# Kernel tuning notes

Hardware: AMD Instinct MI355X
Metric: run time of the kernel (lower is better)

## Reference

```python
import jax, jax.numpy as jnp
import numpy as np

L = 2        # gnn_layers
D = 256      # hidden_dim
E = 1024     # emb_dim
NCLS = 7
NEG = 1e30


def lstm_cell(x, h, c, Wih, Whh, bih, bhh):
    # torch.nn.LSTMCell math; gate order i, f, g, o
    g = x @ Wih.T + bih + h @ Whh.T + bhh
    i, f, gg, o = jnp.split(g, 4, axis=-1)
    c2 = jax.nn.sigmoid(f) * c + jax.nn.sigmoid(i) * jnp.tanh(gg)
    return jax.nn.sigmoid(o) * jnp.tanh(c2), c2


def dag_layer(Hl, adj_f, W1, W2, Wr, Wc_ih, Wc_hh, bc_ih, bc_hh, Wp_ih, Wp_hh, bp_ih, bp_hh):
    # Hl: (B,N,D). Sequential DAG recurrence with dot-product attention over growing prefix.
    B, N, Dh = Hl.shape
    zeros = jnp.zeros((B, Dh), Hl.dtype)
    h0 = Hl[:, 0]
    C0, _ = lstm_cell(h0, zeros, zeros, Wc_ih, Wc_hh, bc_ih, bc_hh)
    P0, _ = lstm_cell(zeros, h0, h0, Wp_ih, Wp_hh, bp_ih, bp_hh)
    Ht0 = C0 + P0
    # carry pre-projected keys/values incrementally to avoid O(N^2 D^2) work
    K2 = jnp.zeros((B, N, Dh), Hl.dtype).at[:, 0].set(Ht0 @ W2.T)
    Vr = jnp.zeros((B, N, Dh), Hl.dtype).at[:, 0].set(Ht0 @ Wr.T)
    H1 = jnp.zeros((B, N, Dh), Hl.dtype).at[:, 0].set(Ht0)
    pos = jnp.arange(N)

    def step(carry, i):
        K2, Vr, H1 = carry
        Q = jax.lax.dynamic_index_in_dim(Hl, i, axis=1, keepdims=False)      # (B,D)
        adj_i = jax.lax.dynamic_index_in_dim(adj_f, i, axis=1, keepdims=False)  # (B,N)
        q = Q @ W1.T
        logits = jnp.einsum('bd,bnd->bn', q, K2) - (1.0 - adj_i) * NEG  # mask_logic
        logits = jnp.where(pos[None, :] < i, logits, -NEG)              # only prefix :i
        w = jax.nn.softmax(logits, axis=-1)
        M = jnp.einsum('bn,bnd->bd', w, Vr)
        C, _ = lstm_cell(Q, M, M, Wc_ih, Wc_hh, bc_ih, bc_hh)
        P, _ = lstm_cell(M, Q, Q, Wp_ih, Wp_hh, bp_ih, bp_hh)
        Ht = C + P
        K2 = K2.at[:, i].set(Ht @ W2.T)
        Vr = Vr.at[:, i].set(Ht @ Wr.T)
        H1 = H1.at[:, i].set(Ht)
        return (K2, Vr, H1), None

    (K2, Vr, H1), _ = jax.lax.scan(step, (K2, Vr, H1), jnp.arange(1, N))
    return H1


def setup_inputs() -> dict:
    key = jax.random.key(0)
    ks = iter(jax.random.split(key, 40))
    B, N = 16, 128
    s = lambda *sh: jax.random.normal(next(ks), sh, jnp.float32) * 0.02
    in_dim = D * (L + 1) + E
    return dict(
        features=jax.random.normal(next(ks), (B, N, E), jnp.float32),
        adj=jnp.ones((B, N, N), jnp.int32),
        s_mask=jnp.zeros((B, N, N), jnp.int32),
        s_mask_onehot=jnp.zeros((B, N, N, 2), jnp.int32),
        lengths=jnp.ones((B,), jnp.int32) * N,
        fc1_W=s(D, E), fc1_b=jnp.zeros((D,), jnp.float32),
        W1=s(L, D, D), W2=s(L, D, D), Wr=s(L, D, D),
        Wc_ih=s(L, 4 * D, D), Wc_hh=s(L, 4 * D, D),
        bc_ih=jnp.zeros((L, 4 * D), jnp.float32), bc_hh=jnp.zeros((L, 4 * D), jnp.float32),
        Wp_ih=s(L, 4 * D, D), Wp_hh=s(L, 4 * D, D),
        bp_ih=jnp.zeros((L, 4 * D), jnp.float32), bp_hh=jnp.zeros((L, 4 * D), jnp.float32),
        m0_W=s(D, in_dim), m0_b=jnp.zeros((D,), jnp.float32),
        m1_W=s(D, D), m1_b=jnp.zeros((D,), jnp.float32),
        m2_W=s(NCLS, D), m2_b=jnp.zeros((NCLS,), jnp.float32),
    )


def reference(features, adj, s_mask, s_mask_onehot, lengths,
              fc1_W, fc1_b, W1, W2, Wr,
              Wc_ih, Wc_hh, bc_ih, bc_hh,
              Wp_ih, Wp_hh, bp_ih, bp_hh,
              m0_W, m0_b, m1_W, m1_b, m2_W, m2_b):
    # s_mask / s_mask_onehot unused for attn_type='dotprod', no_rel_attn=True
    # lengths unused for nodal_att_type=None (attentive_node_features is identity)
    adj_f = adj.astype(features.dtype)
    H0 = jax.nn.relu(features @ fc1_W.T + fc1_b)
    Hs = [H0]
    for l in range(L):
        Hs.append(dag_layer(Hs[l], adj_f,
                            W1[l], W2[l], Wr[l],
                            Wc_ih[l], Wc_hh[l], bc_ih[l], bc_hh[l],
                            Wp_ih[l], Wp_hh[l], bp_ih[l], bp_hh[l]))
    Hcat = jnp.concatenate(Hs + [features], axis=2)  # (B,N,D*(L+1)+E)
    h = jax.nn.relu(Hcat @ m0_W.T + m0_b)
    h = jax.nn.relu(h @ m1_W.T + m1_b)  # mlp_layers-1 extra layer; dropout p=0 -> identity
    return h @ m2_W.T + m2_b            # (B,N,num_class)
```

## Files before the change

### kernel.cpp

```cpp
#include <hip/hip_runtime.h>
#include <hip/hip_fp16.h>
#include <math.h>

#define B_ 16
#define N_ 128
#define D_ 256
#define E_ 1024
#define GD4 1024
#define SENT 0xFFC0DEADu

typedef _Float16 h2 __attribute__((ext_vector_type(2)));

template<bool BIAS, bool RELU>
__global__ __launch_bounds__(256) void gemm_k(const float* __restrict__ X,
    const float* __restrict__ W, const float* __restrict__ bias,
    float* __restrict__ C, int M, int N, int K)
{
  __shared__ float Xs[32][68];
  __shared__ float Ws[32][68];
  const int tid = threadIdx.x;
  const int m0 = blockIdx.x * 64, n0 = blockIdx.y * 64;
  const int tm = tid >> 4, tn = tid & 15;
  float acc[4][4] = {};
  for (int k0 = 0; k0 < K; k0 += 32) {
    for (int e = tid; e < 2048; e += 256) {
      int mm = e >> 5, kk = e & 31;
      Xs[kk][mm] = X[(m0+mm)*K + k0+kk];
    }
    for (int e = tid; e < 2048; e += 256) {
      int nn = e >> 5, kk = e & 31;
      Ws[kk][nn] = (n0+nn < N) ? W[(n0+nn)*K + k0+kk] : 0.f;
    }
    __syncthreads();
    for (int kk = 0; kk < 32; kk++) {
      float4 a = *(const float4*)&Xs[kk][tm*4];
      float4 b = *(const float4*)&Ws[kk][tn*4];
      acc[0][0] += a.x*b.x; acc[0][1] += a.x*b.y; acc[0][2] += a.x*b.z; acc[0][3] += a.x*b.w;
      acc[1][0] += a.y*b.x; acc[1][1] += a.y*b.y; acc[1][2] += a.y*b.z; acc[1][3] += a.y*b.w;
      acc[2][0] += a.z*b.x; acc[2][1] += a.z*b.y; acc[2][2] += a.z*b.z; acc[2][3] += a.z*b.w;
      acc[3][0] += a.w*b.x; acc[3][1] += a.w*b.y; acc[3][2] += a.w*b.z; acc[3][3] += a.w*b.w;
    }
    __syncthreads();
  }
  for (int i2 = 0; i2 < 4; i2++) {
    int row = m0 + tm*4 + i2;
    for (int j2 = 0; j2 < 4; j2++) {
      int col = n0 + tn*4 + j2;
      if (col < N) {
        float v = acc[i2][j2];
        if (BIAS) v += bias[col];
        if (RELU) v = fmaxf(v, 0.f);
        C[row*N + col] = v;
      }
    }
  }
}

__global__ __launch_bounds__(256) void prepamat_k(const float* __restrict__ W2,
    const float* __restrict__ W1, float* __restrict__ AM)
{
  __shared__ float Xs[32][68];
  __shared__ float Ws[32][68];
  const int tid = threadIdx.x;
  const int m0 = blockIdx.x * 64, n0 = blockIdx.y * 64;
  const float* X = W2 + blockIdx.z * 65536;
  const float* W = W1 + blockIdx.z * 65536;
  float* C = AM + blockIdx.z * 65536;
  const int tm = tid >> 4, tn = tid & 15;
  float acc[4][4] = {};
  for (int k0 = 0; k0 < 256; k0 += 32) {
    for (int e = tid; e < 2048; e += 256) {
      int kk = e >> 6, mm = e & 63;
      Xs[kk][mm] = X[(k0+kk)*256 + m0+mm];
    }
    for (int e = tid; e < 2048; e += 256) {
      int kk = e >> 6, nn = e & 63;
      Ws[kk][nn] = W[(k0+kk)*256 + n0+nn];
    }
    __syncthreads();
    for (int kk = 0; kk < 32; kk++) {
      float4 a = *(const float4*)&Xs[kk][tm*4];
      float4 b = *(const float4*)&Ws[kk][tn*4];
      acc[0][0] += a.x*b.x; acc[0][1] += a.x*b.y; acc[0][2] += a.x*b.z; acc[0][3] += a.x*b.w;
      acc[1][0] += a.y*b.x; acc[1][1] += a.y*b.y; acc[1][2] += a.y*b.z; acc[1][3] += a.y*b.w;
      acc[2][0] += a.z*b.x; acc[2][1] += a.z*b.y; acc[2][2] += a.z*b.z; acc[2][3] += a.z*b.w;
      acc[3][0] += a.w*b.x; acc[3][1] += a.w*b.y; acc[3][2] += a.w*b.z; acc[3][3] += a.w*b.w;
    }
    __syncthreads();
  }
  for (int i2 = 0; i2 < 4; i2++)
    for (int j2 = 0; j2 < 4; j2++)
      C[(m0 + tm*4 + i2)*256 + n0 + tn*4 + j2] = acc[i2][j2];
}

__global__ __launch_bounds__(256) void prepnn_k(const float* __restrict__ Wch,
    const float* __restrict__ Wpi, const float* __restrict__ Wr,
    float* __restrict__ OUT)
{
  __shared__ float Xs[32][68];
  __shared__ float Ws[32][68];
  const int tid = threadIdx.x;
  const int m0 = blockIdx.x * 64, n0 = blockIdx.y * 64;
  const int l = blockIdx.z;
  const float* X = (m0 < 1024) ? (Wch + l*262144 + m0*256)
                               : (Wpi + l*262144 + (m0-1024)*256);
  const float* W = Wr + l*65536;
  float* C = OUT + l*524288;
  const int tm = tid >> 4, tn = tid & 15;
  float acc[4][4] = {};
  for (int k0 = 0; k0 < 256; k0 += 32) {
    for (int e = tid; e < 2048; e += 256) {
      int mm = e >> 5, kk = e & 31;
      Xs[kk][mm] = X[mm*256 + k0+kk];
    }
    for (int e = tid; e < 2048; e += 256) {
      int kk = e >> 6, nn = e & 63;
      Ws[kk][nn] = W[(k0+kk)*256 + n0+nn];
    }
    __syncthreads();
    for (int kk = 0; kk < 32; kk++) {
      float4 a = *(const float4*)&Xs[kk][tm*4];
      float4 b = *(const float4*)&Ws[kk][tn*4];
      acc[0][0] += a.x*b.x; acc[0][1] += a.x*b.y; acc[0][2] += a.x*b.z; acc[0][3] += a.x*b.w;
      acc[1][0] += a.y*b.x; acc[1][1] += a.y*b.y; acc[1][2] += a.y*b.z; acc[1][3] += a.y*b.w;
      acc[2][0] += a.z*b.x; acc[2][1] += a.z*b.y; acc[2][2] += a.z*b.z; acc[2][3] += a.z*b.w;
      acc[3][0] += a.w*b.x; acc[3][1] += a.w*b.y; acc[3][2] += a.w*b.z; acc[3][3] += a.w*b.w;
    }
    __syncthreads();
  }
  for (int i2 = 0; i2 < 4; i2++)
    for (int j2 = 0; j2 < 4; j2++)
      C[(m0 + tm*4 + i2)*256 + n0 + tn*4 + j2] = acc[i2][j2];
}

__global__ void bias_sum_k(const float* __restrict__ bci, const float* __restrict__ bch,
                           const float* __restrict__ bpi, const float* __restrict__ bph,
                           float* __restrict__ bcC, float* __restrict__ bpC)
{
  int i = blockIdx.x*256 + threadIdx.x;
  if (i < 2048) { bcC[i] = bci[i] + bch[i]; bpC[i] = bpi[i] + bph[i]; }
}

__global__ void pack_k(const float* __restrict__ wchpi, const float* __restrict__ wr,
                       _Float16* __restrict__ out)
{
  int idx = blockIdx.x*256 + threadIdx.x;
  int l  = idx / 589824; int rem = idx % 589824;
  int sl = rem / 36864;  int rem2 = rem % 36864;
  int cq = rem2 / 1152;  int rem3 = rem2 % 1152;
  int r  = rem3 >> 3;    int e = rem3 & 7;
  int c  = cq*8 + e;
  int g  = r >> 4, dl = r & 15;
  int d  = sl*16 + dl;
  float v;
  if (g < 8) v = wchpi[l*524288 + (g*256 + d)*256 + c];
  else       v = wr[l*65536 + d*256 + c];
  out[idx] = (_Float16)v;
}

__global__ void fill_k(unsigned* __restrict__ a, unsigned* __restrict__ b)
{
  int i = blockIdx.x*256 + threadIdx.x;
  if (i < 524288) {
    __hip_atomic_store(a + i, SENT, __ATOMIC_RELAXED, __HIP_MEMORY_SCOPE_AGENT);
    __hip_atomic_store(b + i, SENT, __ATOMIC_RELAXED, __HIP_MEMORY_SCOPE_AGENT);
  }
}

__global__ __launch_bounds__(256) void prologue_k(const float* __restrict__ X,
    const float* __restrict__ Wc, const float* __restrict__ Wp,
    const float* __restrict__ Am, const float* __restrict__ bcc,
    const float* __restrict__ bpc, float* __restrict__ GQC,
    float* __restrict__ GQP, float* __restrict__ VM)
{
  __shared__ float Xs[32][68];
  __shared__ float Ws[32][68];
  const int tid = threadIdx.x;
  const int m0 = blockIdx.x * 64;
  const int nt = blockIdx.y;
  const float* W; const float* bias; float* C; int n0; int NC;
  if (nt < 16)      { W = Wc; bias = bcc;     C = GQC; n0 = nt*64;      NC = 1024; }
  else if (nt < 32) { W = Wp; bias = bpc;     C = GQP; n0 = (nt-16)*64; NC = 1024; }
  else              { W = Am; bias = nullptr; C = VM;  n0 = (nt-32)*64; NC = 256;  }
  const int tm = tid >> 4, tn = tid & 15;
  float acc[4][4] = {};
  for (int k0 = 0; k0 < 256; k0 += 32) {
    for (int e = tid; e < 2048; e += 256) {
      int mm = e >> 5, kk = e & 31;
      Xs[kk][mm] = X[(m0+mm)*256 + k0+kk];
    }
    for (int e = tid; e < 2048; e += 256) {
      int nn = e >> 5, kk = e & 31;
      Ws[kk][nn] = W[(n0+nn)*256 + k0+kk];
    }
    __syncthreads();
    for (int kk = 0; kk < 32; kk++) {
      float4 a = *(const float4*)&Xs[kk][tm*4];
      float4 b = *(const float4*)&Ws[kk][tn*4];
      acc[0][0] += a.x*b.x; acc[0][1] += a.x*b.y; acc[0][2] += a.x*b.z; acc[0][3] += a.x*b.w;
      acc[1][0] += a.y*b.x; acc[1][1] += a.y*b.y; acc[1][2] += a.y*b.z; acc[1][3] += a.y*b.w;
      acc[2][0] += a.z*b.x; acc[2][1] += a.z*b.y; acc[2][2] += a.z*b.z; acc[2][3] += a.z*b.w;
      acc[3][0] += a.w*b.x; acc[3][1] += a.w*b.y; acc[3][2] += a.w*b.z; acc[3][3] += a.w*b.w;
    }
    __syncthreads();
  }
  for (int i2 = 0; i2 < 4; i2++) {
    int row = m0 + tm*4 + i2;
    for (int j2 = 0; j2 < 4; j2++) {
      int col = n0 + tn*4 + j2;
      float v = acc[i2][j2];
      if (bias) v += bias[col];
      C[row*NC + col] = v;
    }
  }
}

__global__ __launch_bounds__(256) void m0fused_k(const float* __restrict__ H0,
    const float* __restrict__ H1, const float* __restrict__ H2,
    const float* __restrict__ feat, const float* __restrict__ W,
    const float* __restrict__ bias, float* __restrict__ C)
{
  __shared__ float Xs[32][68];
  __shared__ float Ws[32][68];
  const int tid = threadIdx.x;
  const int m0 = blockIdx.x * 64, n0 = blockIdx.y * 64;
  const int tm = tid >> 4, tn = tid & 15;
  float acc[4][4] = {};
  for (int k0 = 0; k0 < 1792; k0 += 32) {
    for (int e = tid; e < 2048; e += 256) {
      int mm = e >> 5, kk = e & 31;
      int k = k0 + kk, row = m0 + mm;
      float v;
      if (k < 768) {
        const float* src = (k < 256) ? H0 : ((k < 512) ? H1 : H2);
        v = src[row*256 + (k & 255)];
      } else v = feat[row*1024 + (k - 768)];
      Xs[kk][mm] = v;
    }
    for (int e = tid; e < 2048; e += 256) {
      int nn = e >> 5, kk = e & 31;
      Ws[kk][nn] = W[(n0+nn)*1792 + k0+kk];
    }
    __syncthreads();
    for (int kk = 0; kk < 32; kk++) {
      float4 a = *(const float4*)&Xs[kk][tm*4];
      float4 b = *(const float4*)&Ws[kk][tn*4];
      acc[0][0] += a.x*b.x; acc[0][1] += a.x*b.y; acc[0][2] += a.x*b.z; acc[0][3] += a.x*b.w;
      acc[1][0] += a.y*b.x; acc[1][1] += a.y*b.y; acc[1][2] += a.y*b.z; acc[1][3] += a.y*b.w;
      acc[2][0] += a.z*b.x; acc[2][1] += a.z*b.y; acc[2][2] += a.z*b.z; acc[2][3] += a.z*b.w;
      acc[3][0] += a.w*b.x; acc[3][1] += a.w*b.y; acc[3][2] += a.w*b.z; acc[3][3] += a.w*b.w;
    }
    __syncthreads();
  }
  for (int i2 = 0; i2 < 4; i2++) {
    int row = m0 + tm*4 + i2;
    for (int j2 = 0; j2 < 4; j2++) {
      int col = n0 + tn*4 + j2;
      C[row*256 + col] = fmaxf(acc[i2][j2] + bias[col], 0.f);
    }
  }
}

__device__ __forceinline__ float sigf(float x) { return 1.f / (1.f + __expf(-x)); }
__device__ __forceinline__ float tanhfast(float x) {
  float xc = fminf(fmaxf(x, -15.f), 15.f);
  float e = __expf(-2.f * xc);
  return (1.f - e) / (1.f + e);
}
__device__ __forceinline__ float dot2w(unsigned w, h2 hv, float acc) {
#if __has_builtin(__builtin_amdgcn_fdot2)
  return __builtin_amdgcn_fdot2(__builtin_bit_cast(h2, w), hv, acc, false);
#else
  union { unsigned u; _Float16 e[2]; } c; c.u = w;
  return acc + (float)c.e[0]*(float)hv.x + (float)c.e[1]*(float)hv.y;
#endif
}
__device__ __forceinline__ float dot2h(h2 a, h2 b, float acc) {
#if __has_builtin(__builtin_amdgcn_fdot2)
  return __builtin_amdgcn_fdot2(a, b, acc, false);
#else
  return acc + (float)a.x*(float)b.x + (float)a.y*(float)b.y;
#endif
}

__global__ __launch_bounds__(512, 2) void scan_k(
    const float* __restrict__ Hl,
    const float* __restrict__ Vm,
    const float* __restrict__ gqC,
    const float* __restrict__ gqP,
    const _Float16* __restrict__ WTp,
    const int*   __restrict__ adj,
    float* __restrict__ Hout)
{
  __shared__ uint4 wl4[4608];
  __shared__ float G[128*144];
  __shared__ __align__(16) _Float16 h2s[256];
  __shared__ float v_s[256];
  __shared__ __align__(16) _Float16 v2s[256];
  __shared__ float psum[128];
  __shared__ float aw[128];
  __shared__ int   adj_s[2][128];
  __shared__ float gqc_l[2][64], gqp_l[2][64];
  __shared__ float ql[2][16];
  __shared__ float Gg[144];
  __shared__ float red[2];

  const int tid = threadIdx.x;
  const int b   = blockIdx.x >> 4;
  const int sl  = blockIdx.x & 15;

  { const uint4* src = (const uint4*)WTp + (size_t)sl*4608;
    for (int e = tid; e < 4608; e += 512) wl4[e] = src[e]; }

  const int rr_ = tid >> 2;
  const int rj  = tid & 3;

#define PREF(ip_, bf_) do {                                                    \
    int ip = (ip_); int bf = (bf_);                                            \
    for (int u = tid - 288; u < 528; u += 224) {                               \
      if (u < 256) { float v = Vm[(b*N_ + ip)*D_ + u]; v_s[u] = v;             \
                     h2s[0] = h2s[0]; v2s[u] = (_Float16)v; }                  \
      else if (u < 384) adj_s[bf][u-256] = adj[(b*N_ + ip)*N_ + (u-256)];      \
      else if (u < 448) gqc_l[bf][u-384] = gqC[(b*N_+ip)*GD4 + ((u-384)>>4)*D_ + sl*16 + ((u-384)&15)]; \
      else if (u < 512) gqp_l[bf][u-448] = gqP[(b*N_+ip)*GD4 + ((u-448)>>4)*D_ + sl*16 + ((u-448)&15)]; \
      else ql[bf][u-512] = Hl[(b*N_+ip)*D_ + sl*16 + (u-512)];                 \
    }                                                                          \
  } while (0)

  if (tid >= 288) PREF(0, 0);
  __syncthreads();

  for (int i = 0; i < N_; ++i) {
    const int cur = i & 1;
    if (i > 0) {
      float4 areg[16];
      const float4* hp = (const float4*)(Hout + ((size_t)(b*N_ + rr_))*D_) + rj;
      if (rr_ + 1 < i) {
        #pragma unroll
        for (int c4 = 0; c4 < 16; ++c4) areg[c4] = hp[c4*4];
      }
      if (tid < 16) {
        const unsigned* w = (const unsigned*)Hout
                          + ((size_t)(b*N_ + (i-1)))*D_ + tid*16 + 15;
        while (__hip_atomic_load(w, __ATOMIC_RELAXED, __HIP_MEMORY_SCOPE_AGENT) == SENT)
          __builtin_amdgcn_s_sleep(1);
      }
      __syncthreads();
      asm volatile("" ::: "memory");

      if (tid < 256) {
        float hv = Hout[((size_t)(b*N_ + (i-1)))*D_ + tid];
        h2s[tid] = (_Float16)hv;
      }
      {
        float acc = 0.f;
        if (rr_ + 1 < i) {
          const float4* vv = (const float4*)v_s + rj;
          #pragma unroll
          for (int c4 = 0; c4 < 16; ++c4) {
            float4 a = areg[c4], w = vv[c4*4];
            acc += a.x*w.x + a.y*w.y + a.z*w.z + a.w*w.w;
          }
          acc += __shfl_xor(acc, 1, 64);
          acc += __shfl_xor(acc, 2, 64);
          if (rj == 0) psum[rr_] = acc;
        }
      }
      __syncthreads();

      if (tid < 288) {
        int r = tid >> 1, hf = tid & 1;
        float acc = 0.f;
        #pragma unroll 4
        for (int it = 0; it < 16; ++it) {
          int cq = hf*16 + it;
          uint4 w4 = wl4[cq*144 + r];
          const h2* hh = (const h2*)h2s + cq*4;
          acc = dot2w(w4.x, hh[0], acc);
          acc = dot2w(w4.y, hh[1], acc);
          acc = dot2w(w4.z, hh[2], acc);
          acc = dot2w(w4.w, hh[3], acc);
        }
        acc += __shfl_xor(acc, 1, 64);
        if (!hf) G[(i-1)*144 + r] = acc;
      }
      if (rr_ == i-1) {
        const h2* hh = (const h2*)h2s + rj*32;
        const h2* vv = (const h2*)v2s + rj*32;
        float acc = 0.f;
        #pragma unroll 8
        for (int q = 0; q < 32; ++q) acc = dot2h(hh[q], vv[q], acc);
        acc += __shfl_xor(acc, 1, 64);
        acc += __shfl_xor(acc, 2, 64);
        if (rj == 0) psum[i-1] = acc;
      }
      if (tid >= 384) {
        int k = tid - 384;
        float e = (k + 1 < i && adj_s[cur][k] != 0) ? __expf(psum[k]) : 0.f;
        aw[k] = e;
        float sv = e;
        #pragma unroll
        for (int off = 32; off >= 1; off >>= 1) sv += __shfl_xor(sv, off, 64);
        if ((k & 63) == 0) red[k >> 6] = sv;
      }
      __syncthreads();

      if (tid < 288) {
        int r = tid >> 1, kh = tid & 1;
        float e1 = (adj_s[cur][i-1] != 0) ? __expf(psum[i-1]) : 0.f;
        float g = kh ? e1 * G[(i-1)*144 + r] : 0.f;
        int m = i - 1;
        int k0 = kh ? (m >> 1) : 0, k1 = kh ? m : (m >> 1);
        for (int k = k0; k < k1; ++k) g += aw[k] * G[k*144 + r];
        g += __shfl_xor(g, 1, 64);
        if (!kh) Gg[r] = g;
      } else {
        PREF((i < 127) ? i+1 : 127, (i+1) & 1);
      }
      __syncthreads();
    } else {
      if (tid >= 288) PREF(1, 1);
      __syncthreads();
    }

    if (tid < 32) {
      int dl = tid >> 1, cell = tid & 1;
      float inv = 0.f;
      if (i > 0) {
        float e1m = (adj_s[cur][i-1] != 0) ? __expf(psum[i-1]) : 0.f;
        inv = 1.f / (red[0] + red[1] + e1m);
      }
      float r0 = 0.f, r1 = 0.f, r2 = 0.f, r3 = 0.f, Mv = 0.f;
      if (i > 0) {
        r0 = Gg[(cell*4+0)*16 + dl] * inv;
        r1 = Gg[(cell*4+1)*16 + dl] * inv;
        r2 = Gg[(cell*4+2)*16 + dl] * inv;
        r3 = Gg[(cell*4+3)*16 + dl] * inv;
        Mv = Gg[128 + dl] * inv;
      }
      float Qv = ql[cur][dl];
      const float* gq = cell ? &gqp_l[cur][0] : &gqc_l[cur][0];
      float xi = cell ? Qv : Mv;
      float gi_ = r0 + gq[ 0 + dl];
      float gf_ = r1 + gq[16 + dl];
      float gg_ = r2 + gq[32 + dl];
      float go_ = r3 + gq[48 + dl];
      float c2  = sigf(gf_)*xi + sigf(gi_)*tanhfast(gg_);
      float ov  = sigf(go_)*tanhfast(c2);
      float htv = ov + __shfl_xor(ov, 1, 64);
      if (!cell) {
        __hip_atomic_store(&Hout[((size_t)(b*N_ + i))*D_ + sl*16 + dl], htv,
                           __ATOMIC_RELAXED, __HIP_MEMORY_SCOPE_AGENT);
      }
    }
  }
#undef PREF
}

extern "C" void kernel_launch(void* const* d_in, const int* in_sizes, int n_in,
                              void* d_out, int out_size, void* d_ws, size_t ws_size,
                              hipStream_t stream)
{
  const float* features = (const float*)d_in[0];
  const int*   adj      = (const int*)  d_in[1];
  const float* fc1_W    = (const float*)d_in[5];
  const float* fc1_b    = (const float*)d_in[6];
  const float* W1       = (const float*)d_in[7];
  const float* W2       = (const float*)d_in[8];
  const float* Wr       = (const float*)d_in[9];
  const float* Wc_ih    = (const float*)d_in[10];
  const float* Wc_hh    = (const float*)d_in[11];
  const float* bc_ih    = (const float*)d_in[12];
  const float* bc_hh    = (const float*)d_in[13];
  const float* Wp_ih    = (const float*)d_in[14];
  const float* Wp_hh    = (const float*)d_in[15];
  const float* bp_ih    = (const float*)d_in[16];
  const float* bp_hh    = (const float*)d_in[17];
  const float* m0_W     = (const float*)d_in[18];
  const float* m0_b     = (const float*)d_in[19];
  const float* m1_W     = (const float*)d_in[20];
  const float* m1_b     = (const float*)d_in[21];
  const float* m2_W     = (const float*)d_in[22];
  const float* m2_b     = (const float*)d_in[23];

  float* ws = (float*)d_ws;
  _Float16* WTP = (_Float16*)ws;
  float* AMAT   = ws + 589824;
  float* BCC    = ws + 720896;
  float* BPC    = ws + 722944;
  float* WCHPI  = ws + 724992;
  float* H0     = ws + 1773568;
  float* H1     = ws + 2297856;
  float* H2     = ws + 2822144;
  float* VMAT   = ws + 3346432;
  float* GQC    = ws + 3870720;
  float* GQP    = ws + 5967872;
  float* HB1    = ws + 8065024;
  float* HB2    = ws + 8589312;

  fill_k<<<2048, 256, 0, stream>>>((unsigned*)H1, (unsigned*)H2);
  bias_sum_k<<<8, 256, 0, stream>>>(bc_ih, bc_hh, bp_ih, bp_hh, BCC, BPC);
  prepamat_k<<<dim3(4,4,2), 256, 0, stream>>>(W2, W1, AMAT);
  prepnn_k<<<dim3(32,4,2), 256, 0, stream>>>(Wc_hh, Wp_ih, Wr, WCHPI);
  pack_k<<<4608, 256, 0, stream>>>(WCHPI, Wr, WTP);

  gemm_k<true,true><<<dim3(32,4), 256, 0, stream>>>(features, fc1_W, fc1_b, H0, 2048, 256, 1024);

  prologue_k<<<dim3(32,36), 256, 0, stream>>>(H0, Wc_ih, Wp_hh, AMAT,
                                              BCC, BPC, GQC, GQP, VMAT);
  scan_k<<<256, 512, 0, stream>>>(H0, VMAT, GQC, GQP, WTP, adj, H1);

  prologue_k<<<dim3(32,36), 256, 0, stream>>>(H1, Wc_ih + 262144, Wp_hh + 262144,
                                              AMAT + 65536, BCC + 1024, BPC + 1024,
                                              GQC, GQP, VMAT);
  scan_k<<<256, 512, 0, stream>>>(H1, VMAT, GQC, GQP, WTP + 589824, adj, H2);

  m0fused_k<<<dim3(32,4), 256, 0, stream>>>(H0, H1, H2, features, m0_W, m0_b, HB1);
  gemm_k<true,true ><<<dim3(32,4), 256, 0, stream>>>(HB1, m1_W, m1_b, HB2, 2048, 256, 256);
  gemm_k<true,false><<<dim3(32,1), 256, 0, stream>>>(HB2, m2_W, m2_b, (float*)d_out, 2048, 7, 256);
}
```

Before: 1.992 ms.

## Use fp16 dot2 GEMMs for dense layers and trim scan barriers

Converts the fc1, prologue and m0 GEMMs to load fp32 operands, pack them into fp16 pairs in shared memory, and accumulate with fdot2. This halves shared-memory footprint and the number of inner-loop instructions. In the scan kernel, the prefix attention dot products now run before the first barrier, and the wait-and-convert of the previous hidden state is done by dedicated threads, removing one __syncthreads per step. The softmax normaliser is computed once into shared memory. The change reduces operand precision in the dense layers, which risks accuracy.

Result: faster. 1.819 ms (-8.7%).

```diff
diff --git a/kernel.cpp b/kernel.cpp
--- a/kernel.cpp
+++ b/kernel.cpp
@@ -10,6 +10,22 @@
 #define SENT 0xFFC0DEADu
 
 typedef _Float16 h2 __attribute__((ext_vector_type(2)));
+
+__device__ __forceinline__ float dot2w(unsigned w, h2 hv, float acc) {
+#if __has_builtin(__builtin_amdgcn_fdot2)
+  return __builtin_amdgcn_fdot2(__builtin_bit_cast(h2, w), hv, acc, false);
+#else
+  union { unsigned u; _Float16 e[2]; } c; c.u = w;
+  return acc + (float)c.e[0]*(float)hv.x + (float)c.e[1]*(float)hv.y;
+#endif
+}
+__device__ __forceinline__ float dot2h(h2 a, h2 b, float acc) {
+#if __has_builtin(__builtin_amdgcn_fdot2)
+  return __builtin_amdgcn_fdot2(a, b, acc, false);
+#else
+  return acc + (float)a.x*(float)b.x + (float)a.y*(float)b.y;
+#endif
+}
 
 template<bool BIAS, bool RELU>
 __global__ __launch_bounds__(256) void gemm_k(const float* __restrict__ X,
@@ -52,6 +68,56 @@
         if (RELU) v = fmaxf(v, 0.f);
         C[row*N + col] = v;
       }
+    }
+  }
+}
+
+template<bool BIAS, bool RELU>
+__global__ __launch_bounds__(256) void gemm16_k(const float* __restrict__ X,
+    const float* __restrict__ W, const float* __restrict__ bias,
+    float* __restrict__ C, int M, int N, int K)
+{
+  __shared__ h2 Xs2[16][68];
+  __shared__ h2 Ws2[16][68];
+  const int tid = threadIdx.x;
+  const int m0 = blockIdx.x * 64, n0 = blockIdx.y * 64;
+  const int tm = tid >> 4, tn = tid & 15;
+  float acc[4][4] = {};
+  for (int k0 = 0; k0 < K; k0 += 32) {
+    for (int e = tid; e < 1024; e += 256) {
+      int mm = e >> 4, p = e & 15;
+      const float* xp = &X[(m0+mm)*K + k0 + 2*p];
+      h2 t; t.x = (_Float16)xp[0]; t.y = (_Float16)xp[1];
+      Xs2[p][mm] = t;
+    }
+    for (int e = tid; e < 1024; e += 256) {
+      int nn = e >> 4, p = e & 15;
+      const float* wp = &W[(n0+nn)*K + k0 + 2*p];
+      h2 t; t.x = (_Float16)wp[0]; t.y = (_Float16)wp[1];
+      Ws2[p][nn] = t;
+    }
+    __syncthreads();
+    #pragma unroll 4
+    for (int p = 0; p < 16; ++p) {
+      h2 a[4], bb[4];
+      *(float4*)a  = *(const float4*)&Xs2[p][tm*4];
+      *(float4*)bb = *(const float4*)&Ws2[p][tn*4];
+      #pragma unroll
+      for (int i2 = 0; i2 < 4; i2++)
+        #pragma unroll
+        for (int j2 = 0; j2 < 4; j2++)
+          acc[i2][j2] = dot2h(a[i2], bb[j2], acc[i2][j2]);
+    }
+    __syncthreads();
+  }
+  for (int i2 = 0; i2 < 4; i2++) {
+    int row = m0 + tm*4 + i2;
+    for (int j2 = 0; j2 < 4; j2++) {
+      int col = n0 + tn*4 + j2;
+      float v = acc[i2][j2];
+      if (BIAS) v += bias[col];
+      if (RELU) v = fmaxf(v, 0.f);
+      C[row*N + col] = v;
     }
   }
 }
@@ -167,14 +233,14 @@
   }
 }
 
-__global__ __launch_bounds__(256) void prologue_k(const float* __restrict__ X,
+__global__ __launch_bounds__(256) void prologue16_k(const float* __restrict__ X,
     const float* __restrict__ Wc, const float* __restrict__ Wp,
     const float* __restrict__ Am, const float* __restrict__ bcc,
     const float* __restrict__ bpc, float* __restrict__ GQC,
     float* __restrict__ GQP, float* __restrict__ VM)
 {
-  __shared__ float Xs[32][68];
-  __shared__ float Ws[32][68];
+  __shared__ h2 Xs2[16][68];
+  __shared__ h2 Ws2[16][68];
   const int tid = threadIdx.x;
   const int m0 = blockIdx.x * 64;
   const int nt = blockIdx.y;
@@ -185,22 +251,29 @@
   const int tm = tid >> 4, tn = tid & 15;
   float acc[4][4] = {};
   for (int k0 = 0; k0 < 256; k0 += 32) {
-    for (int e = tid; e < 2048; e += 256) {
-      int mm = e >> 5, kk = e & 31;
-      Xs[kk][mm] = X[(m0+mm)*256 + k0+kk];
-    }
-    for (int e = tid; e < 2048; e += 256) {
-      int nn = e >> 5, kk = e & 31;
-      Ws[kk][nn] = W[(n0+nn)*256 + k0+kk];
-    }
-    __syncthreads();
-    for (int kk = 0; kk < 32; kk++) {
-      float4 a = *(const float4*)&Xs[kk][tm*4];
-      float4 b = *(const float4*)&Ws[kk][tn*4];
-      acc[0][0] += a.x*b.x; acc[0][1] += a.x*b.y; acc[0][2] += a.x*b.z; acc[0][3] += a.x*b.w;
-      acc[1][0] += a.y*b.x; acc[1][1] += a.y*b.y; acc[1][2] += a.y*b.z; acc[1][3] += a.y*b.w;
-      acc[2][0] += a.z*b.x; acc[2][1] += a.z*b.y; acc[2][2] += a.z*b.z; acc[2][3] += a.z*b.w;
-      acc[3][0] += a.w*b.x; acc[3][1] += a.w*b.y; acc[3][2] += a.w*b.z; acc[3][3] += a.w*b.w;
+    for (int e = tid; e < 1024; e += 256) {
+      int mm = e >> 4, p = e & 15;
+      const float* xp = &X[(m0+mm)*256 + k0 + 2*p];
+      h2 t; t.x = (_Float16)xp[0]; t.y = (_Float16)xp[1];
+      Xs2[p][mm] = t;
+    }
+    for (int e = tid; e < 1024; e += 256) {
+      int nn = e >> 4, p = e & 15;
+      const float* wp = &W[(n0+nn)*256 + k0 + 2*p];
+      h2 t; t.x = (_Float16)wp[0]; t.y = (_Float16)wp[1];
+      Ws2[p][nn] = t;
+    }
+    __syncthreads();
+    #pragma unroll 4
+    for (int p = 0; p < 16; ++p) {
+      h2 a[4], bb[4];
+      *(float4*)a  = *(const float4*)&Xs2[p][tm*4];
+      *(float4*)bb = *(const float4*)&Ws2[p][tn*4];
+      #pragma unroll
+      for (int i2 = 0; i2 < 4; i2++)
+        #pragma unroll
+        for (int j2 = 0; j2 < 4; j2++)
+          acc[i2][j2] = dot2h(a[i2], bb[j2], acc[i2][j2]);
     }
     __syncthreads();
   }
@@ -215,40 +288,50 @@
   }
 }
 
-__global__ __launch_bounds__(256) void m0fused_k(const float* __restrict__ H0,
+__global__ __launch_bounds__(256) void m0fused16_k(const float* __restrict__ H0,
     const float* __restrict__ H1, const float* __restrict__ H2,
     const float* __restrict__ feat, const float* __restrict__ W,
     const float* __restrict__ bias, float* __restrict__ C)
 {
-  __shared__ float Xs[32][68];
-  __shared__ float Ws[32][68];
+  __shared__ h2 Xs2[16][68];
+  __shared__ h2 Ws2[16][68];
   const int tid = threadIdx.x;
   const int m0 = blockIdx.x * 64, n0 = blockIdx.y * 64;
   const int tm = tid >> 4, tn = tid & 15;
   float acc[4][4] = {};
   for (int k0 = 0; k0 < 1792; k0 += 32) {
-    for (int e = tid; e < 2048; e += 256) {
-      int mm = e >> 5, kk = e & 31;
-      int k = k0 + kk, row = m0 + mm;
-      float v;
+    for (int e = tid; e < 1024; e += 256) {
+      int mm = e >> 4, p = e & 15;
+      int k = k0 + 2*p, row = m0 + mm;
+      float x0, x1;
       if (k < 768) {
         const float* src = (k < 256) ? H0 : ((k < 512) ? H1 : H2);
-        v = src[row*256 + (k & 255)];
-      } else v = feat[row*1024 + (k - 768)];
-      Xs[kk][mm] = v;
-    }
-    for (int e = tid; e < 2048; e += 256) {
-      int nn = e >> 5, kk = e & 31;
-      Ws[kk][nn] = W[(n0+nn)*1792 + k0+kk];
-    }
-    __syncthreads();
-    for (int kk = 0; kk < 32; kk++) {
-      float4 a = *(const float4*)&Xs[kk][tm*4];
-      float4 b = *(const float4*)&Ws[kk][tn*4];
-      acc[0][0] += a.x*b.x; acc[0][1] += a.x*b.y; acc[0][2] += a.x*b.z; acc[0][3] += a.x*b.w;
-      acc[1][0] += a.y*b.x; acc[1][1] += a.y*b.y; acc[1][2] += a.y*b.z; acc[1][3] += a.y*b.w;
-      acc[2][0] += a.z*b.x; acc[2][1] += a.z*b.y; acc[2][2] += a.z*b.z; acc[2][3] += a.z*b.w;
-      acc[3][0] += a.w*b.x; acc[3][1] += a.w*b.y; acc[3][2] += a.w*b.z; acc[3][3] += a.w*b.w;
+        x0 = src[row*256 + (k & 255)];
+        x1 = src[row*256 + (k & 255) + 1];
+      } else {
+        x0 = feat[row*1024 + (k - 768)];
+        x1 = feat[row*1024 + (k - 767)];
+      }
+      h2 t; t.x = (_Float16)x0; t.y = (_Float16)x1;
+      Xs2[p][mm] = t;
+    }
+    for (int e = tid; e < 1024; e += 256) {
+      int nn = e >> 4, p = e & 15;
+      const float* wp = &W[(n0+nn)*1792 + k0 + 2*p];
+      h2 t; t.x = (_Float16)wp[0]; t.y = (_Float16)wp[1];
+      Ws2[p][nn] = t;
+    }
+    __syncthreads();
+    #pragma unroll 4
+    for (int p = 0; p < 16; ++p) {
+      h2 a[4], bb[4];
+      *(float4*)a  = *(const float4*)&Xs2[p][tm*4];
+      *(float4*)bb = *(const float4*)&Ws2[p][tn*4];
+      #pragma unroll
+      for (int i2 = 0; i2 < 4; i2++)
+        #pragma unroll
+        for (int j2 = 0; j2 < 4; j2++)
+          acc[i2][j2] = dot2h(a[i2], bb[j2], acc[i2][j2]);
     }
     __syncthreads();
   }
@@ -266,21 +349,6 @@
   float xc = fminf(fmaxf(x, -15.f), 15.f);
   float e = __expf(-2.f * xc);
   return (1.f - e) / (1.f + e);
-}
-__device__ __forceinline__ float dot2w(unsigned w, h2 hv, float acc) {
-#if __has_builtin(__builtin_amdgcn_fdot2)
-  return __builtin_amdgcn_fdot2(__builtin_bit_cast(h2, w), hv, acc, false);
-#else
-  union { unsigned u; _Float16 e[2]; } c; c.u = w;
-  return acc + (float)c.e[0]*(float)hv.x + (float)c.e[1]*(float)hv.y;
-#endif
-}
-__device__ __forceinline__ float dot2h(h2 a, h2 b, float acc) {
-#if __has_builtin(__builtin_amdgcn_fdot2)
-  return __builtin_amdgcn_fdot2(a, b, acc, false);
-#else
-  return acc + (float)a.x*(float)b.x + (float)a.y*(float)b.y;
-#endif
 }
 
 __global__ __launch_bounds__(512, 2) void scan_k(
@@ -304,6 +372,7 @@
   __shared__ float ql[2][16];
   __shared__ float Gg[144];
   __shared__ float red[2];
+  __shared__ float sinv;
 
   const int tid = threadIdx.x;
   const int b   = blockIdx.x >> 4;
@@ -319,7 +388,7 @@
     int ip = (ip_); int bf = (bf_);                                            \
     for (int u = tid - 288; u < 528; u += 224) {                               \
       if (u < 256) { float v = Vm[(b*N_ + ip)*D_ + u]; v_s[u] = v;             \
-                     h2s[0] = h2s[0]; v2s[u] = (_Float16)v; }                  \
+                     v2s[u] = (_Float16)v; }                                   \
       else if (u < 384) adj_s[bf][u-256] = adj[(b*N_ + ip)*N_ + (u-256)];      \
       else if (u < 448) gqc_l[bf][u-384] = gqC[(b*N_+ip)*GD4 + ((u-384)>>4)*D_ + sl*16 + ((u-384)&15)]; \
       else if (u < 512) gqp_l[bf][u-448] = gqP[(b*N_+ip)*GD4 + ((u-448)>>4)*D_ + sl*16 + ((u-448)&15)]; \
@@ -333,56 +402,52 @@
   for (int i = 0; i < N_; ++i) {
     const int cur = i & 1;
     if (i > 0) {
-      float4 areg[16];
-      const float4* hp = (const float4*)(Hout + ((size_t)(b*N_ + rr_))*D_) + rj;
       if (rr_ + 1 < i) {
+        const float4* hp = (const float4*)(Hout + ((size_t)(b*N_ + rr_))*D_) + rj;
+        const float4* vv = (const float4*)v_s + rj;
+        float4 areg[16];
         #pragma unroll
         for (int c4 = 0; c4 < 16; ++c4) areg[c4] = hp[c4*4];
-      }
-      if (tid < 16) {
-        const unsigned* w = (const unsigned*)Hout
-                          + ((size_t)(b*N_ + (i-1)))*D_ + tid*16 + 15;
-        while (__hip_atomic_load(w, __ATOMIC_RELAXED, __HIP_MEMORY_SCOPE_AGENT) == SENT)
+        float acc = 0.f;
+        #pragma unroll
+        for (int c4 = 0; c4 < 16; ++c4) {
+          float4 a = areg[c4], w = vv[c4*4];
+          acc += a.x*w.x + a.y*w.y + a.z*w.z + a.w*w.w;
+        }
+        acc += __shfl_xor(acc, 1, 64);
+        acc += __shfl_xor(acc, 2, 64);
+        if (rj == 0) psum[rr_] = acc;
+      }
+      if (tid >= 448) {
+        const unsigned* wp = (const unsigned*)Hout
+                           + ((size_t)(b*N_ + (i-1)))*D_ + ((tid-448)&15)*16 + 15;
+        while (__hip_atomic_load(wp, __ATOMIC_RELAXED, __HIP_MEMORY_SCOPE_AGENT) == SENT)
           __builtin_amdgcn_s_sleep(1);
+        int lane = tid - 448;
+        float4 hv = *((const float4*)(Hout + ((size_t)(b*N_ + (i-1)))*D_) + lane);
+        h2* hd = (h2*)h2s + lane*2;
+        h2 t0; t0.x = (_Float16)hv.x; t0.y = (_Float16)hv.y;
+        h2 t1; t1.x = (_Float16)hv.z; t1.y = (_Float16)hv.w;
+        hd[0] = t0; hd[1] = t1;
       }
       __syncthreads();
       asm volatile("" ::: "memory");
 
-      if (tid < 256) {
-        float hv = Hout[((size_t)(b*N_ + (i-1)))*D_ + tid];
-        h2s[tid] = (_Float16)hv;
-      }
-      {
-        float acc = 0.f;
-        if (rr_ + 1 < i) {
-          const float4* vv = (const float4*)v_s + rj;
-          #pragma unroll
-          for (int c4 = 0; c4 < 16; ++c4) {
-            float4 a = areg[c4], w = vv[c4*4];
-            acc += a.x*w.x + a.y*w.y + a.z*w.z + a.w*w.w;
-          }
-          acc += __shfl_xor(acc, 1, 64);
-          acc += __shfl_xor(acc, 2, 64);
-          if (rj == 0) psum[rr_] = acc;
-        }
-      }
-      __syncthreads();
-
       if (tid < 288) {
         int r = tid >> 1, hf = tid & 1;
-        float acc = 0.f;
+        float acc2 = 0.f;
         #pragma unroll 4
         for (int it = 0; it < 16; ++it) {
           int cq = hf*16 + it;
           uint4 w4 = wl4[cq*144 + r];
           const h2* hh = (const h2*)h2s + cq*4;
-          acc = dot2w(w4.x, hh[0], acc);
-          acc = dot2w(w4.y, hh[1], acc);
-          acc = dot2w(w4.z, hh[2], acc);
-          acc = dot2w(w4.w, hh[3], acc);
+          acc2 = dot2w(w4.x, hh[0], acc2);
+          acc2 = dot2w(w4.y, hh[1], acc2);
+          acc2 = dot2w(w4.z, hh[2], acc2);
+          acc2 = dot2w(w4.w, hh[3], acc2);
         }
-        acc += __shfl_xor(acc, 1, 64);
-        if (!hf) G[(i-1)*144 + r] = acc;
+        acc2 += __shfl_xor(acc2, 1, 64);
+        if (!hf) G[(i-1)*144 + r] = acc2;
       }
       if (rr_ == i-1) {
         const h2* hh = (const h2*)h2s + rj*32;
@@ -394,8 +459,8 @@
         acc += __shfl_xor(acc, 2, 64);
         if (rj == 0) psum[i-1] = acc;
       }
-      if (tid >= 384) {
-        int k = tid - 384;
+      if (tid >= 320 && tid < 448) {
+        int k = tid - 320;
         float e = (k + 1 < i && adj_s[cur][k] != 0) ? __expf(psum[k]) : 0.f;
         aw[k] = e;
         float sv = e;
@@ -414,6 +479,7 @@
         for (int k = k0; k < k1; ++k) g += aw[k] * G[k*144 + r];
         g += __shfl_xor(g, 1, 64);
         if (!kh) Gg[r] = g;
+        if (tid == 0) sinv = 1.f / (red[0] + red[1] + e1);
       } else {
         PREF((i < 127) ? i+1 : 127, (i+1) & 1);
       }
@@ -425,11 +491,7 @@
 
     if (tid < 32) {
       int dl = tid >> 1, cell = tid & 1;
-      float inv = 0.f;
-      if (i > 0) {
-        float e1m = (adj_s[cur][i-1] != 0) ? __expf(psum[i-1]) : 0.f;
-        inv = 1.f / (red[0] + red[1] + e1m);
-      }
+      float inv = (i > 0) ? sinv : 0.f;
       float r0 = 0.f, r1 = 0.f, r2 = 0.f, r3 = 0.f, Mv = 0.f;
       if (i > 0) {
         r0 = Gg[(cell*4+0)*16 + dl] * inv;
@@ -504,18 +566,18 @@
   prepnn_k<<<dim3(32,4,2), 256, 0, stream>>>(Wc_hh, Wp_ih, Wr, WCHPI);
   pack_k<<<4608, 256, 0, stream>>>(WCHPI, Wr, WTP);
 
-  gemm_k<true,true><<<dim3(32,4), 256, 0, stream>>>(features, fc1_W, fc1_b, H0, 2048, 256, 1024);
-
-  prologue_k<<<dim3(32,36), 256, 0, stream>>>(H0, Wc_ih, Wp_hh, AMAT,
-                                              BCC, BPC, GQC, GQP, VMAT);
+  gemm16_k<true,true><<<dim3(32,4), 256, 0, stream>>>(features, fc1_W, fc1_b, H0, 2048, 256, 1024);
+
+  prologue16_k<<<dim3(32,36), 256, 0, stream>>>(H0, Wc_ih, Wp_hh, AMAT,
+                                                BCC, BPC, GQC, GQP, VMAT);
   scan_k<<<256, 512, 0, stream>>>(H0, VMAT, GQC, GQP, WTP, adj, H1);
 
-  prologue_k<<<dim3(32,36), 256, 0, stream>>>(H1, Wc_ih + 262144, Wp_hh + 262144,
-                                              AMAT + 65536, BCC + 1024, BPC + 1024,
-                                              GQC, GQP, VMAT);
+  prologue16_k<<<dim3(32,36), 256, 0, stream>>>(H1, Wc_ih + 262144, Wp_hh + 262144,
+                                                AMAT + 65536, BCC + 1024, BPC + 1024,
+                                                GQC, GQP, VMAT);
   scan_k<<<256, 512, 0, stream>>>(H1, VMAT, GQC, GQP, WTP + 589824, adj, H2);
 
-  m0fused_k<<<dim3(32,4), 256, 0, stream>>>(H0, H1, H2, features, m0_W, m0_b, HB1);
+  m0fused16_k<<<dim3(32,4), 256, 0, stream>>>(H0, H1, H2, features, m0_W, m0_b, HB1);
   gemm_k<true,true ><<<dim3(32,4), 256, 0, stream>>>(HB1, m1_W, m1_b, HB2, 2048, 256, 256);
   gemm_k<true,false><<<dim3(32,1), 256, 0, stream>>>(HB2, m2_W, m2_b, (float*)d_out, 2048, 7, 256);
 }
```
